# Performance work log

Hardware: AMD Instinct MI355X
Metric: run time of the kernel (lower is better)

The kernel has to match this reference:

```python
import jax, jax.numpy as jnp
import numpy as np

B, N, D, H = 4, 2048, 1024, 16
DH = D // H


def setup_inputs() -> dict:
    key = jax.random.key(0)
    ks = jax.random.split(key, 9)
    std = 0.02
    return {
        "x": jax.random.normal(ks[0], (B, N, D), dtype=jnp.float32),
        "Wq": jax.random.normal(ks[1], (D, D), dtype=jnp.float32) * std,
        "bq": jnp.zeros((D,), dtype=jnp.float32),
        "Wk": jax.random.normal(ks[2], (D, D), dtype=jnp.float32) * std,
        "bk": jnp.zeros((D,), dtype=jnp.float32),
        "Wv": jax.random.normal(ks[3], (D, D), dtype=jnp.float32) * std,
        "bv": jnp.zeros((D,), dtype=jnp.float32),
        "Wo": jax.random.normal(ks[4], (D, D), dtype=jnp.float32) * std,
        "bo": jnp.zeros((D,), dtype=jnp.float32),
        "k": 8,
        "dilation": 2,
    }


def _dilated_mask(n_q, n_k, k, dilation):
    # allowed[i, j] = True iff |j - i| <= k*dilation and (j - i) % dilation == 0
    i = jnp.arange(n_q)[:, None]
    j = jnp.arange(n_k)[None, :]
    d = j - i
    return (jnp.abs(d) <= k * dilation) & ((d % dilation) == 0)


def reference(x, Wq, bq, Wk, bk, Wv, bv, Wo, bo, k, dilation):
    b, n_q, d_model = x.shape
    n_heads = H
    d_head = d_model // n_heads
    # self-attention: context = x
    q = (x @ Wq + bq).reshape(b, n_q, n_heads, d_head).transpose(0, 2, 1, 3)  # (B,H,Nq,Dh)
    kk = (x @ Wk + bk).reshape(b, n_q, n_heads, d_head).transpose(0, 2, 1, 3)
    v = (x @ Wv + bv).reshape(b, n_q, n_heads, d_head).transpose(0, 2, 1, 3)

    scale = 1.0 / np.sqrt(d_head).astype(np.float32)
    scores = jnp.einsum("bhqd,bhkd->bhqk", q, kk) * scale  # (B,H,Nq,Nk)
    allowed = _dilated_mask(n_q, n_q, k, dilation)  # (Nq,Nk)
    scores = jnp.where(allowed[None, None], scores, -jnp.inf)
    attn = jax.nn.softmax(scores, axis=-1)
    out = jnp.einsum("bhqk,bhkd->bhqd", attn, v)  # (B,H,Nq,Dh)
    out = out.transpose(0, 2, 1, 3).reshape(b, n_q, d_model)
    return out @ Wo + bo
```

## Files before the change

kernel.cpp:

```cpp
#include <hip/hip_runtime.h>
#include <hip/hip_bf16.h>
#include <hip/hip_fp16.h>
#include <stdint.h>

using bf16 = __hip_bfloat16;

typedef __bf16    bf16x8 __attribute__((ext_vector_type(8)));
typedef float     floatx4 __attribute__((ext_vector_type(4)));
typedef _Float16  f16x2 __attribute__((ext_vector_type(2)));
typedef _Float16  f16x8 __attribute__((ext_vector_type(8)));

typedef __attribute__((address_space(3))) void as3_void;
typedef __attribute__((address_space(1))) void as1_void;

#define GLD_LDS16(gp, lp) \
  __builtin_amdgcn_global_load_lds((as1_void*)(uintptr_t)(gp), (as3_void*)(uintptr_t)(lp), 16, 0, 0)

#if __has_builtin(__builtin_amdgcn_fdot2)
#define DOT2(a, b, c) __builtin_amdgcn_fdot2((a), (b), (c), false)
#else
#define DOT2(a, b, c) ((c) + (float)(a)[0] * (float)(b)[0] + (float)(a)[1] * (float)(b)[1])
#endif

__global__ __launch_bounds__(256) void convert_x_kernel(const float* __restrict__ x,
                                                        bf16* __restrict__ xbf) {
  const int i = (blockIdx.x * 256 + threadIdx.x) * 4;
  const float4 v = *(const float4*)(x + i);
  bf16 o[4] = {(bf16)v.x, (bf16)v.y, (bf16)v.z, (bf16)v.w};
  *(ushort4*)(xbf + i) = *(const ushort4*)o;
}

__global__ void transpose_w_kernel(const float* __restrict__ Wq, const float* __restrict__ Wk,
                                   const float* __restrict__ Wv, const float* __restrict__ Wo,
                                   bf16* __restrict__ WTqkv, bf16* __restrict__ WoT) {
  __shared__ float tile[32][33];
  const int z = blockIdx.z;
  const float* src = (z == 0) ? Wq : (z == 1) ? Wk : (z == 2) ? Wv : Wo;
  bf16* dst = (z < 3) ? (WTqkv + (size_t)z * 1024 * 1024) : WoT;
  const int tx = threadIdx.x, ty = threadIdx.y;
  const int nbase = blockIdx.x * 32, kbase = blockIdx.y * 32;
#pragma unroll
  for (int r = 0; r < 32; r += 8)
    tile[ty + r][tx] = src[(size_t)(kbase + ty + r) * 1024 + nbase + tx];
  __syncthreads();
#pragma unroll
  for (int r = 0; r < 32; r += 8)
    dst[(size_t)(nbase + ty + r) * 1024 + kbase + tx] = (bf16)tile[tx][ty + r];
}

template <int MODE>
__global__ __launch_bounds__(256) void gemm_bt_kernel(
    const bf16* __restrict__ A, const bf16* __restrict__ Bt,
    const float* __restrict__ b0, const float* __restrict__ b1, const float* __restrict__ b2,
    __half* __restrict__ out0, __half* __restrict__ out1, __half* __restrict__ out2,
    float* __restrict__ fout) {
  const int tid  = threadIdx.x;
  const int m0   = blockIdx.x * 128;
  const int n0   = blockIdx.y * 128;
  const int lane = tid & 63;
  const int wave = tid >> 6;
  const int wr   = (wave >> 1) * 64;
  const int wc   = (wave & 1) * 64;
  const int quad = lane >> 4;
  const int l16  = lane & 15;

  __shared__ alignas(16) bf16 As[128 * 64];
  __shared__ alignas(16) bf16 Bs[128 * 64];

  const int srow = tid >> 3;
  const int scol = (((tid & 7) ^ (srow & 7)) << 3);
  const uint64_t aoff = (uint64_t)(m0 + srow) * 1024 + scol;
  const uint64_t boff = (uint64_t)(n0 + srow) * 1024 + scol;

  floatx4 acc[4][4];
#pragma unroll
  for (int i = 0; i < 4; ++i)
#pragma unroll
    for (int j = 0; j < 4; ++j) {
      floatx4 z = {0.f, 0.f, 0.f, 0.f};
      acc[i][j] = z;
    }

  for (int k0 = 0; k0 < 1024; k0 += 64) {
    __syncthreads();
#pragma unroll
    for (int it = 0; it < 4; ++it) {
      GLD_LDS16(A  + aoff + (uint64_t)it * 32768 + k0, (char*)As + it * 4096 + tid * 16);
      GLD_LDS16(Bt + boff + (uint64_t)it * 32768 + k0, (char*)Bs + it * 4096 + tid * 16);
    }
    __syncthreads();

#pragma unroll
    for (int kc = 0; kc < 2; ++kc) {
      bf16x8 af[4], bfr[4];
#pragma unroll
      for (int i = 0; i < 4; ++i) {
        const int mrow = wr + i * 16 + l16;
        const int pca  = (kc * 4 + quad) ^ (mrow & 7);
        af[i] = *(const bf16x8*)(As + mrow * 64 + pca * 8);
        const int nrow = wc + i * 16 + l16;
        const int pcb  = (kc * 4 + quad) ^ (nrow & 7);
        bfr[i] = *(const bf16x8*)(Bs + nrow * 64 + pcb * 8);
      }
#pragma unroll
      for (int i = 0; i < 4; ++i)
#pragma unroll
        for (int j = 0; j < 4; ++j)
          acc[i][j] = __builtin_amdgcn_mfma_f32_16x16x32_bf16(af[i], bfr[j], acc[i][j], 0, 0, 0);
    }
  }

#pragma unroll
  for (int i = 0; i < 4; ++i) {
#pragma unroll
    for (int j = 0; j < 4; ++j) {
#pragma unroll
      for (int r = 0; r < 4; ++r) {
        const int m = m0 + wr + i * 16 + quad * 4 + r;
        const int n = n0 + wc + j * 16 + l16;
        float v = acc[i][j][r];
        if (MODE == 0) {
          const int which = n >> 10;
          const int c = n & 1023;
          const float* bp = (which == 0) ? b0 : (which == 1) ? b1 : b2;
          __half* op      = (which == 0) ? out0 : (which == 1) ? out1 : out2;
          v += bp[c];
          const int h = c >> 6, dh = c & 63;
          const int bb = m >> 11, seq = m & 2047;
          op[(uint64_t)(bb * 16 + h) * 131072 + (uint64_t)seq * 64 + dh] = (__half)v;
        } else {
          fout[(uint64_t)m * 1024 + n] = v + b0[n];
        }
      }
    }
  }
}

#define RMAX 32
#define RSTRIDE 66

#define ATTN_T_BODY(PTR_K, PTR_V, ROWOFF)                                  \
  {                                                                        \
    f16x8 kc[8];                                                           \
    _Pragma("unroll")                                                      \
    for (int c = 0; c < 8; ++c)                                            \
      kc[c] = *(const f16x8*)((PTR_K) + (ROWOFF) + c * 8);                 \
    float sp[4] = {0.f, 0.f, 0.f, 0.f};                                    \
    _Pragma("unroll")                                                      \
    for (int c = 0; c < 8; ++c) {                                          \
      _Pragma("unroll")                                                    \
      for (int u = 0; u < 4; ++u) {                                        \
        const f16x2 qa = {q[c][2 * u], q[c][2 * u + 1]};                   \
        const f16x2 ka = {kc[c][2 * u], kc[c][2 * u + 1]};                 \
        sp[c & 3] = DOT2(qa, ka, sp[c & 3]);                               \
      }                                                                    \
    }                                                                      \
    const float s = (sp[0] + sp[1]) + (sp[2] + sp[3]);                     \
    const float pe = valid ? __expf(s * 0.125f) : 0.f;                     \
    l += pe;                                                               \
    const _Float16 ph = (_Float16)pe;                                      \
    const f16x2 pe2 = {ph, ph};                                            \
    _Pragma("unroll")                                                      \
    for (int c = 0; c < 8; ++c) {                                          \
      const f16x8 vc = *(const f16x8*)((PTR_V) + (ROWOFF) + c * 8);        \
      _Pragma("unroll")                                                    \
      for (int u = 0; u < 4; ++u) {                                        \
        const f16x2 va = {vc[2 * u], vc[2 * u + 1]};                       \
        oo[c * 4 + u] += pe2 * va;                                         \
      }                                                                    \
    }                                                                      \
  }

__global__ __launch_bounds__(128) void dilated_attn_kernel(
    const __half* __restrict__ Q, const __half* __restrict__ K, const __half* __restrict__ V,
    bf16* __restrict__ attn_out, const int* __restrict__ kptr, const int* __restrict__ dptr) {
  const int tid = threadIdx.x;
  const int bh  = blockIdx.x >> 4;
  const int qb  = blockIdx.x & 15;
  const int Q0  = qb * 128;
  const int kk  = kptr[0];
  const int dil = dptr[0];
  const int R   = kk * dil;

  const size_t base = (size_t)bh * 2048 * 64;

  __shared__ alignas(16) _Float16 Ks[192 * RSTRIDE];
  __shared__ alignas(16) _Float16 Vs[192 * RSTRIDE];

  const int jlo_b = (Q0 - RMAX > 0) ? Q0 - RMAX : 0;
  const int jhi_b = (Q0 + 127 + RMAX < 2047) ? Q0 + 127 + RMAX : 2047;
  const int nrows = jhi_b - jlo_b + 1;
  const bool fast = (R <= RMAX) && (dil > 0);

  if (fast) {
    const int nch = nrows * 8;
    for (int c = tid; c < nch; c += 128) {
      const int r = c >> 3, ch = (c & 7) * 8;
      const size_t g = base + (size_t)(jlo_b + r) * 64 + ch;
      *(f16x8*)(Ks + r * RSTRIDE + ch) = *(const f16x8*)((const _Float16*)K + g);
      *(f16x8*)(Vs + r * RSTRIDE + ch) = *(const f16x8*)((const _Float16*)V + g);
    }
    __syncthreads();
  }

  const int wave = tid >> 6, lane = tid & 63;
  const int i = Q0 + wave * 64 + lane;

  f16x8 q[8];
#pragma unroll
  for (int t = 0; t < 8; ++t)
    q[t] = *(const f16x8*)((const _Float16*)Q + base + (size_t)i * 64 + t * 8);

  float l = 0.f;
  f16x2 oo[32];
#pragma unroll
  for (int t = 0; t < 32; ++t) oo[t] = (f16x2){(_Float16)0, (_Float16)0};

  if (fast) {
    const int rbase = i - jlo_b;
    for (int t = -kk; t <= kk; ++t) {
      const int j = i + t * dil;
      const bool valid = (unsigned)j < 2048u;
      int row = rbase + t * dil;
      row = (row < 0) ? 0 : (row >= nrows ? nrows - 1 : row);
      const int rowoff = row * RSTRIDE;
      ATTN_T_BODY(Ks, Vs, rowoff)
    }
  } else {
    for (int t = -kk; t <= kk; ++t) {
      const int j = i + t * dil;
      const bool valid = (unsigned)j < 2048u;
      const int jc = valid ? j : i;
      const size_t rowoff = base + (size_t)jc * 64;
      ATTN_T_BODY((const _Float16*)K, (const _Float16*)V, rowoff)
    }
  }

  const float linv = 1.f / fmaxf(l, 1e-30f);
  const int bb = bh >> 4, h = bh & 15;
  alignas(16) bf16 orow[64];
#pragma unroll
  for (int t = 0; t < 32; ++t) {
    orow[2 * t]     = (bf16)((float)oo[t][0] * linv);
    orow[2 * t + 1] = (bf16)((float)oo[t][1] * linv);
  }
  bf16* dst = attn_out + ((size_t)(bb * 2048 + i) * 1024 + h * 64);
#pragma unroll
  for (int c = 0; c < 8; ++c)
    *(uint4*)(dst + c * 8) = *(const uint4*)(orow + c * 8);
}

extern "C" void kernel_launch(void* const* d_in, const int* in_sizes, int n_in,
                              void* d_out, int out_size, void* d_ws, size_t ws_size,
                              hipStream_t stream) {
  const float* x  = (const float*)d_in[0];
  const float* Wq = (const float*)d_in[1];
  const float* bq = (const float*)d_in[2];
  const float* Wk = (const float*)d_in[3];
  const float* bk = (const float*)d_in[4];
  const float* Wv = (const float*)d_in[5];
  const float* bv = (const float*)d_in[6];
  const float* Wo = (const float*)d_in[7];
  const float* bo = (const float*)d_in[8];
  const int* kp   = (const int*)d_in[9];
  const int* dp   = (const int*)d_in[10];
  float* out = (float*)d_out;

  bf16*   xbf   = (bf16*)d_ws;
  bf16*   WTqkv = xbf + 8388608;
  bf16*   WoT   = WTqkv + 3072 * 1024;
  __half* qbuf  = (__half*)(WoT + 1024 * 1024);
  __half* kbuf  = qbuf + 8388608;
  __half* vbuf  = kbuf + 8388608;
  bf16*   attn  = xbf;

  convert_x_kernel<<<dim3(8192), 256, 0, stream>>>(x, xbf);
  transpose_w_kernel<<<dim3(32, 32, 4), dim3(32, 8), 0, stream>>>(Wq, Wk, Wv, Wo, WTqkv, WoT);

  gemm_bt_kernel<0><<<dim3(64, 24), 256, 0, stream>>>(xbf, WTqkv, bq, bk, bv,
                                                      qbuf, kbuf, vbuf, nullptr);

  dilated_attn_kernel<<<dim3(1024), 128, 0, stream>>>(qbuf, kbuf, vbuf, attn, kp, dp);

  gemm_bt_kernel<1><<<dim3(64, 8), 256, 0, stream>>>(attn, WoT, bo, nullptr, nullptr,
                                                     nullptr, nullptr, nullptr, out);
}
```

Before: 219.4 us.

## Write attention output head-major, read V from global, widen weight transpose tiles

```diff
diff --git a/kernel.cpp b/kernel.cpp
--- a/kernel.cpp
+++ b/kernel.cpp
@@ -30,22 +30,35 @@
   *(ushort4*)(xbf + i) = *(const ushort4*)o;
 }
 
-__global__ void transpose_w_kernel(const float* __restrict__ Wq, const float* __restrict__ Wk,
-                                   const float* __restrict__ Wv, const float* __restrict__ Wo,
-                                   bf16* __restrict__ WTqkv, bf16* __restrict__ WoT) {
-  __shared__ float tile[32][33];
+__global__ __launch_bounds__(256) void transpose_w_kernel(
+    const float* __restrict__ Wq, const float* __restrict__ Wk,
+    const float* __restrict__ Wv, const float* __restrict__ Wo,
+    bf16* __restrict__ WTqkv, bf16* __restrict__ WoT) {
+  __shared__ float tile[64 * 68];
   const int z = blockIdx.z;
   const float* src = (z == 0) ? Wq : (z == 1) ? Wk : (z == 2) ? Wv : Wo;
   bf16* dst = (z < 3) ? (WTqkv + (size_t)z * 1024 * 1024) : WoT;
-  const int tx = threadIdx.x, ty = threadIdx.y;
-  const int nbase = blockIdx.x * 32, kbase = blockIdx.y * 32;
-#pragma unroll
-  for (int r = 0; r < 32; r += 8)
-    tile[ty + r][tx] = src[(size_t)(kbase + ty + r) * 1024 + nbase + tx];
+  const int tid = threadIdx.x;
+  const int nbase = blockIdx.x * 64, kbase = blockIdx.y * 64;
+
+  const int r1 = tid >> 4, c1 = tid & 15;
+#pragma unroll
+  for (int it = 0; it < 4; ++it) {
+    const int row = r1 + it * 16;
+    const float4 v = *(const float4*)(src + (size_t)(kbase + row) * 1024 + nbase + c1 * 4);
+    *(float4*)(tile + row * 68 + c1 * 4) = v;
+  }
   __syncthreads();
-#pragma unroll
-  for (int r = 0; r < 32; r += 8)
-    dst[(size_t)(nbase + ty + r) * 1024 + kbase + tx] = (bf16)tile[tx][ty + r];
+
+  const int c2 = tid & 7, n2 = tid >> 3;
+#pragma unroll
+  for (int it2 = 0; it2 < 2; ++it2) {
+    const int n = n2 + it2 * 32;
+    bf16 o[8];
+#pragma unroll
+    for (int s = 0; s < 8; ++s) o[s] = (bf16)tile[(8 * c2 + s) * 68 + n];
+    *(uint4*)(dst + (size_t)(nbase + n) * 1024 + kbase + 8 * c2) = *(const uint4*)o;
+  }
 }
 
 template <int MODE>
@@ -68,9 +81,15 @@
   __shared__ alignas(16) bf16 Bs[128 * 64];
 
   const int srow = tid >> 3;
-  const int scol = (((tid & 7) ^ (srow & 7)) << 3);
-  const uint64_t aoff = (uint64_t)(m0 + srow) * 1024 + scol;
-  const uint64_t boff = (uint64_t)(n0 + srow) * 1024 + scol;
+  const int cg   = (tid & 7) ^ (srow & 7);
+  uint64_t aoff;
+  if (MODE == 0) {
+    aoff = (uint64_t)(m0 + srow) * 1024 + cg * 8;
+  } else {
+    const int b = m0 >> 11, seq0 = m0 & 2047;
+    aoff = (uint64_t)b * 2097152 + (uint64_t)(seq0 + srow) * 64 + cg * 8;
+  }
+  const uint64_t boff = (uint64_t)(n0 + srow) * 1024 + cg * 8;
 
   floatx4 acc[4][4];
 #pragma unroll
@@ -85,7 +104,11 @@
     __syncthreads();
 #pragma unroll
     for (int it = 0; it < 4; ++it) {
-      GLD_LDS16(A  + aoff + (uint64_t)it * 32768 + k0, (char*)As + it * 4096 + tid * 16);
+      if (MODE == 0)
+        GLD_LDS16(A + aoff + (uint64_t)it * 32768 + k0, (char*)As + it * 4096 + tid * 16);
+      else
+        GLD_LDS16(A + aoff + (uint64_t)it * 2048 + (uint64_t)(k0 >> 6) * 131072,
+                  (char*)As + it * 4096 + tid * 16);
       GLD_LDS16(Bt + boff + (uint64_t)it * 32768 + k0, (char*)Bs + it * 4096 + tid * 16);
     }
     __syncthreads();
@@ -139,12 +162,15 @@
 #define RMAX 32
 #define RSTRIDE 66
 
-#define ATTN_T_BODY(PTR_K, PTR_V, ROWOFF)                                  \
+#define ATTN_T_BODY(KPTR, KIDX, VPTR)                                      \
   {                                                                        \
+    f16x8 vc[8];                                                           \
+    _Pragma("unroll")                                                      \
+    for (int c = 0; c < 8; ++c) vc[c] = *(const f16x8*)((VPTR) + c * 8);   \
     f16x8 kc[8];                                                           \
     _Pragma("unroll")                                                      \
     for (int c = 0; c < 8; ++c)                                            \
-      kc[c] = *(const f16x8*)((PTR_K) + (ROWOFF) + c * 8);                 \
+      kc[c] = *(const f16x8*)((KPTR) + (KIDX) + c * 8);                    \
     float sp[4] = {0.f, 0.f, 0.f, 0.f};                                    \
     _Pragma("unroll")                                                      \
     for (int c = 0; c < 8; ++c) {                                          \
@@ -162,10 +188,9 @@
     const f16x2 pe2 = {ph, ph};                                            \
     _Pragma("unroll")                                                      \
     for (int c = 0; c < 8; ++c) {                                          \
-      const f16x8 vc = *(const f16x8*)((PTR_V) + (ROWOFF) + c * 8);        \
       _Pragma("unroll")                                                    \
       for (int u = 0; u < 4; ++u) {                                        \
-        const f16x2 va = {vc[2 * u], vc[2 * u + 1]};                       \
+        const f16x2 va = {vc[c][2 * u], vc[c][2 * u + 1]};                 \
         oo[c * 4 + u] += pe2 * va;                                         \
       }                                                                    \
     }                                                                      \
@@ -185,7 +210,6 @@
   const size_t base = (size_t)bh * 2048 * 64;
 
   __shared__ alignas(16) _Float16 Ks[192 * RSTRIDE];
-  __shared__ alignas(16) _Float16 Vs[192 * RSTRIDE];
 
   const int jlo_b = (Q0 - RMAX > 0) ? Q0 - RMAX : 0;
   const int jhi_b = (Q0 + 127 + RMAX < 2047) ? Q0 + 127 + RMAX : 2047;
@@ -196,9 +220,8 @@
     const int nch = nrows * 8;
     for (int c = tid; c < nch; c += 128) {
       const int r = c >> 3, ch = (c & 7) * 8;
-      const size_t g = base + (size_t)(jlo_b + r) * 64 + ch;
-      *(f16x8*)(Ks + r * RSTRIDE + ch) = *(const f16x8*)((const _Float16*)K + g);
-      *(f16x8*)(Vs + r * RSTRIDE + ch) = *(const f16x8*)((const _Float16*)V + g);
+      *(f16x8*)(Ks + r * RSTRIDE + ch) =
+          *(const f16x8*)((const _Float16*)K + base + (size_t)(jlo_b + r) * 64 + ch);
     }
     __syncthreads();
   }
@@ -223,28 +246,27 @@
       const bool valid = (unsigned)j < 2048u;
       int row = rbase + t * dil;
       row = (row < 0) ? 0 : (row >= nrows ? nrows - 1 : row);
-      const int rowoff = row * RSTRIDE;
-      ATTN_T_BODY(Ks, Vs, rowoff)
+      const _Float16* vp = (const _Float16*)V + base + (size_t)(valid ? j : i) * 64;
+      ATTN_T_BODY(Ks, row * RSTRIDE, vp)
     }
   } else {
     for (int t = -kk; t <= kk; ++t) {
       const int j = i + t * dil;
       const bool valid = (unsigned)j < 2048u;
       const int jc = valid ? j : i;
-      const size_t rowoff = base + (size_t)jc * 64;
-      ATTN_T_BODY((const _Float16*)K, (const _Float16*)V, rowoff)
+      const _Float16* vp = (const _Float16*)V + base + (size_t)jc * 64;
+      ATTN_T_BODY((const _Float16*)K, base + (size_t)jc * 64, vp)
     }
   }
 
   const float linv = 1.f / fmaxf(l, 1e-30f);
-  const int bb = bh >> 4, h = bh & 15;
   alignas(16) bf16 orow[64];
 #pragma unroll
   for (int t = 0; t < 32; ++t) {
     orow[2 * t]     = (bf16)((float)oo[t][0] * linv);
     orow[2 * t + 1] = (bf16)((float)oo[t][1] * linv);
   }
-  bf16* dst = attn_out + ((size_t)(bb * 2048 + i) * 1024 + h * 64);
+  bf16* dst = attn_out + base + (size_t)i * 64;
 #pragma unroll
   for (int c = 0; c < 8; ++c)
     *(uint4*)(dst + c * 8) = *(const uint4*)(orow + c * 8);
@@ -272,16 +294,16 @@
   __half* qbuf  = (__half*)(WoT + 1024 * 1024);
   __half* kbuf  = qbuf + 8388608;
   __half* vbuf  = kbuf + 8388608;
-  bf16*   attn  = xbf;
+  bf16*   attnH = xbf;
 
   convert_x_kernel<<<dim3(8192), 256, 0, stream>>>(x, xbf);
-  transpose_w_kernel<<<dim3(32, 32, 4), dim3(32, 8), 0, stream>>>(Wq, Wk, Wv, Wo, WTqkv, WoT);
+  transpose_w_kernel<<<dim3(16, 16, 4), 256, 0, stream>>>(Wq, Wk, Wv, Wo, WTqkv, WoT);
 
   gemm_bt_kernel<0><<<dim3(64, 24), 256, 0, stream>>>(xbf, WTqkv, bq, bk, bv,
                                                       qbuf, kbuf, vbuf, nullptr);
 
-  dilated_attn_kernel<<<dim3(1024), 128, 0, stream>>>(qbuf, kbuf, vbuf, attn, kp, dp);
-
-  gemm_bt_kernel<1><<<dim3(64, 8), 256, 0, stream>>>(attn, WoT, bo, nullptr, nullptr,
+  dilated_attn_kernel<<<dim3(1024), 128, 0, stream>>>(qbuf, kbuf, vbuf, attnH, kp, dp);
+
+  gemm_bt_kernel<1><<<dim3(64, 8), 256, 0, stream>>>(attnH, WoT, bo, nullptr, nullptr,
                                                      nullptr, nullptr, nullptr, out);
 }
```

New measurement: 234.5 us. +6.9%, slower.
